# Kernel optimization log

Measured on AMD Instinct MI355X. Metric: run time of the kernel, lower is better.

Reference implementation:

```python
import jax, jax.numpy as jnp
import numpy as np

# dims
B, S, D, H, L = 4, 2048, 512, 8, 4
DH = D // H          # head dim 64
MLP = 2048
VOCAB = 32000
BLK = 128            # block size
NB = S // BLK        # 16 blocks
SINK_ITERS = 8       # sinkhorn normalization iterations
NEG = -1e9


def _sinusoid_pos_emb(max_len, d):
    pos = np.arange(max_len, dtype=np.float32)[:, None]
    div = np.exp(np.arange(0, d, 2, dtype=np.float32) * (-np.log(10000.0) / d))
    pe = np.zeros((max_len, d), np.float32)
    pe[:, 0::2] = np.sin(pos * div)
    pe[:, 1::2] = np.cos(pos * div)
    return pe

_PE = jnp.asarray(_sinusoid_pos_emb(S, D))


def setup_inputs() -> dict:
    key = jax.random.key(0)
    ks = jax.random.split(key, 12)
    g = lambda k, shape, s=0.02: jax.random.normal(k, shape, jnp.float32) * s
    tokens = jax.random.randint(ks[0], (B, S), 0, VOCAB)
    return {
        "tokens": tokens,
        "embed": g(ks[1], (VOCAB, D), 1.0),
        "ln1_s": jnp.ones((L, D)), "ln1_b": jnp.zeros((L, D)),
        "wq": g(ks[2], (L, D, H, DH)),
        "wk": g(ks[3], (L, D, H, DH)),
        "wv": g(ks[4], (L, D, H, DH)),
        "wo": g(ks[5], (L, H, DH, D)),
        "sort_w": g(ks[6], (L, H, DH, NB)),
        "ln2_s": jnp.ones((L, D)), "ln2_b": jnp.zeros((L, D)),
        "w1": g(ks[7], (L, D, MLP)), "b1": jnp.zeros((L, MLP)),
        "w2": g(ks[8], (L, MLP, D)), "b2": jnp.zeros((L, D)),
        "lnf_s": jnp.ones((D,)), "lnf_b": jnp.zeros((D,)),
    }


def _ln(x, s, b):
    m = jnp.mean(x, axis=-1, keepdims=True)
    v = jnp.mean(jnp.square(x - m), axis=-1, keepdims=True)
    return (x - m) * jax.lax.rsqrt(v + 1e-6) * s + b


def _sinkhorn(log_alpha):
    # iterative row/col normalization in log space -> soft permutation
    for _ in range(SINK_ITERS):
        log_alpha = log_alpha - jax.nn.logsumexp(log_alpha, axis=-1, keepdims=True)
        log_alpha = log_alpha - jax.nn.logsumexp(log_alpha, axis=-2, keepdims=True)
    return jnp.exp(log_alpha)


def _forward(tokens, embed, ln1_s, ln1_b, wq, wk, wv, wo, sort_w,
             ln2_s, ln2_b, w1, b1, w2, b2, lnf_s, lnf_b):
    pad = (tokens > 0)                       # [B,S] key padding mask
    mb = pad.reshape(B, NB, BLK).astype(jnp.float32)  # block mask
    x = embed[tokens] + _PE[None, :S]        # [B,S,D]
    scale = 1.0 / jnp.sqrt(jnp.float32(DH))
    for l in range(L):
        h = _ln(x, ln1_s[l], ln1_b[l])
        q = jnp.einsum('bsd,dhf->bshf', h, wq[l]) * scale
        k = jnp.einsum('bsd,dhf->bshf', h, wk[l])
        v = jnp.einsum('bsd,dhf->bshf', h, wv[l])
        qb = q.reshape(B, NB, BLK, H, DH)
        kb = k.reshape(B, NB, BLK, H, DH)
        vb = v.reshape(B, NB, BLK, H, DH)
        # sort net: block summary of keys -> block-to-block logits per head
        ksum = kb.sum(axis=2)                               # [B,NB,H,DH]
        logits = jnp.einsum('bnhd,hdm->bhnm', ksum, sort_w[l])
        perm = _sinkhorn(logits)                            # [B,H,NB,NB]
        sk = jnp.einsum('bhnm,bmchd->bnchd', perm, kb)      # sorted key blocks
        sv = jnp.einsum('bhnm,bmchd->bnchd', perm, vb)
        kcat = jnp.concatenate([kb, sk], axis=2)            # [B,NB,2BLK,H,DH]
        vcat = jnp.concatenate([vb, sv], axis=2)
        scores = jnp.einsum('bnqhd,bnkhd->bhnqk', qb, kcat)  # [B,H,NB,BLK,2BLK]
        # padding bias: local part from block mask, sorted part via permuted mask
        local = jnp.broadcast_to(mb[:, None, :, None, :], (B, H, NB, 1, BLK))
        smask = (jnp.einsum('bhnm,bmc->bhnc', jax.lax.stop_gradient(perm), mb) > 0.5)
        smask = smask[:, :, :, None, :].astype(jnp.float32)
        full_mask = jnp.concatenate([local, jnp.broadcast_to(smask, (B, H, NB, 1, BLK))], axis=-1)
        scores = scores + jnp.where(full_mask > 0.5, 0.0, NEG)
        attn = jax.nn.softmax(scores, axis=-1)
        o = jnp.einsum('bhnqk,bnkhd->bnqhd', attn, vcat).reshape(B, S, H, DH)
        x = x + jnp.einsum('bshd,hdD->bsD', o, wo[l])
        y = _ln(x, ln2_s[l], ln2_b[l])
        y = jax.nn.gelu(jnp.einsum('bsd,df->bsf', y, w1[l]) + b1[l])
        x = x + jnp.einsum('bsf,fd->bsd', y, w2[l]) + b2[l]
    return _ln(x, lnf_s, lnf_b)


def reference(tokens, embed, ln1_s, ln1_b, wq, wk, wv, wo, sort_w,
              ln2_s, ln2_b, w1, b1, w2, b2, lnf_s, lnf_b):
    return _forward(tokens, embed, ln1_s, ln1_b, wq, wk, wv, wo, sort_w,
                    ln2_s, ln2_b, w1, b1, w2, b2, lnf_s, lnf_b)
```

## Files before the change

### kernel.cpp

```cpp
#include <hip/hip_runtime.h>
#include <math.h>

#define B_ 4
#define S_ 2048
#define D_ 512
#define H_ 8
#define L_ 4
#define DH_ 64
#define MLP_ 2048
#define BLK_ 128
#define NB_ 16
#define NEGINF -1e9f
#define NXE ((size_t)B_ * S_ * D_)

typedef unsigned short u16;
typedef __attribute__((ext_vector_type(8))) short short8;
typedef __attribute__((ext_vector_type(4))) short short4v;
typedef __attribute__((ext_vector_type(4))) float f32x4;

__device__ __forceinline__ float bf2f(u16 s) {
  return __uint_as_float(((unsigned)s) << 16);
}
__device__ __forceinline__ u16 f2bf(float f) {
  unsigned u = __float_as_uint(f);
  unsigned r = (u + 0x7FFFu + ((u >> 16) & 1u)) >> 16;
  return (u16)r;
}

__device__ __forceinline__ void gll16(const void* g, void* l) {
  __builtin_amdgcn_global_load_lds(
      (const __attribute__((address_space(1))) unsigned int*)g,
      (__attribute__((address_space(3))) unsigned int*)l, 16, 0, 0);
}

__global__ __launch_bounds__(128) void k_embed(const int* __restrict__ tokens,
                                               const float* __restrict__ embed,
                                               float* __restrict__ x) {
  int s = blockIdx.x;
  int tid = threadIdx.x;
  const float c = -logf(10000.0f) / (float)D_;
  int d = tid * 4;
  float pe[4];
#pragma unroll
  for (int j = 0; j < 4; ++j) {
    int dd = d + j;
    int i2 = dd >> 1;
    float freq = __expf(c * (float)(2 * i2));
    float ang = (float)s * freq;
    pe[j] = (dd & 1) ? cosf(ang) : sinf(ang);
  }
#pragma unroll
  for (int b = 0; b < B_; ++b) {
    int tok = tokens[b * S_ + s];
    float4 e = *(const float4*)(embed + (size_t)tok * D_ + d);
    *(float4*)(x + (size_t)(b * S_ + s) * D_ + d) =
        make_float4(e.x + pe[0], e.y + pe[1], e.z + pe[2], e.w + pe[3]);
  }
}

template <typename OT>
__global__ __launch_bounds__(256) void k_ln(const float* __restrict__ x,
                                            const float* __restrict__ sc,
                                            const float* __restrict__ bi,
                                            OT* __restrict__ out, int rows) {
  int row = blockIdx.x * 4 + (threadIdx.x >> 6);
  int lane = threadIdx.x & 63;
  if (row >= rows) return;
  const float* xr = x + (size_t)row * D_;
  float v[8];
  float4 a = *(const float4*)(xr + lane * 8);
  float4 b = *(const float4*)(xr + lane * 8 + 4);
  v[0]=a.x; v[1]=a.y; v[2]=a.z; v[3]=a.w; v[4]=b.x; v[5]=b.y; v[6]=b.z; v[7]=b.w;
  float sum = 0.f;
#pragma unroll
  for (int j = 0; j < 8; ++j) sum += v[j];
#pragma unroll
  for (int off = 32; off; off >>= 1) sum += __shfl_xor(sum, off);
  float mean = sum * (1.0f / D_);
  float var = 0.f;
#pragma unroll
  for (int j = 0; j < 8; ++j) { float d = v[j] - mean; var += d * d; }
#pragma unroll
  for (int off = 32; off; off >>= 1) var += __shfl_xor(var, off);
  float rstd = rsqrtf(var * (1.0f / D_) + 1e-6f);
  float o[8];
#pragma unroll
  for (int j = 0; j < 8; ++j) {
    int d = lane * 8 + j;
    o[j] = (v[j] - mean) * rstd * sc[d] + bi[d];
  }
  if constexpr (sizeof(OT) == 4) {
    float* op = (float*)out + (size_t)row * D_ + lane * 8;
    *(float4*)op = make_float4(o[0], o[1], o[2], o[3]);
    *(float4*)(op + 4) = make_float4(o[4], o[5], o[6], o[7]);
  } else {
    u16* op = (u16*)out + (size_t)row * D_ + lane * 8;
    short8 o8;
#pragma unroll
    for (int j = 0; j < 8; ++j) o8[j] = (short)f2bf(o[j]);
    *(short8*)op = o8;
  }
}

__global__ __launch_bounds__(256) void k_transp(const float* __restrict__ W,
                                                u16* __restrict__ WT, int K, int N,
                                                size_t wStrideZ, size_t tStrideZ) {
  __shared__ float t[32][33];
  const float* Wl = W + (size_t)blockIdx.z * wStrideZ;
  u16* WTl = WT + (size_t)blockIdx.z * tStrideZ;
  int k0 = blockIdx.x * 32, n0 = blockIdx.y * 32;
  int x = threadIdx.x & 31, y = threadIdx.x >> 5;
#pragma unroll
  for (int yy = y; yy < 32; yy += 8)
    t[yy][x] = Wl[(size_t)(k0 + yy) * N + n0 + x];
  __syncthreads();
#pragma unroll
  for (int yy = y; yy < 32; yy += 8)
    WTl[(size_t)(n0 + yy) * K + k0 + x] = f2bf(t[x][yy]);
}

__device__ __forceinline__ float gelu_f(float x) {
  float y = 0.7978845608028654f * (x + 0.044715f * x * x * x);
  float e = __expf(2.0f * y);
  return x - x / (e + 1.0f);
}

enum { EPI_STORE = 0, EPI_ADD = 1, EPI_GELU = 2, EPI_ADDBIAS = 3, EPI_QKV = 4 };

template <int EPI>
__device__ __forceinline__ void epilogue_elem(u16* Cb, float* Cf, float bv,
                                              int row, int col, int N, float alpha,
                                              float v) {
  if (EPI == EPI_STORE) {
    Cb[(size_t)row * N + col] = f2bf(v * alpha);
  } else if (EPI == EPI_QKV) {
    u16* dst = Cb + (size_t)(col >> 9) * NXE;
    float al = (col < 512) ? alpha : 1.0f;
    dst[(size_t)row * D_ + (col & 511)] = f2bf(v * al);
  } else if (EPI == EPI_GELU) {
    Cb[(size_t)row * N + col] = f2bf(gelu_f(v + bv));
  } else if (EPI == EPI_ADD) {
    Cf[(size_t)row * N + col] += v;
  } else {
    Cf[(size_t)row * N + col] += v + bv;
  }
}

template <int EPI>
__global__ __launch_bounds__(256) void k_mm(const u16* __restrict__ A,
                                            const u16* __restrict__ BT,
                                            const float* __restrict__ bias,
                                            u16* __restrict__ Cb,
                                            float* __restrict__ Cf,
                                            int M, int N, int K, float alpha) {
  __shared__ u16 Al[2][128 * 32];
  __shared__ u16 Bl[2][128 * 32];
  int tid = threadIdx.x;
  int lane = tid & 63;
  int wave = tid >> 6;
  int nwg = gridDim.x * gridDim.y;
  int bid = blockIdx.y * gridDim.x + blockIdx.x;
  int cpx = nwg >> 3;
  int swz = (bid & 7) * cpx + (bid >> 3);
  int bx = swz % gridDim.x, by = swz / gridDim.x;
  int m0 = by * 128, n0 = bx * 128;
  int wm = (wave >> 1) * 64, wn = (wave & 1) * 64;
  int l15 = lane & 15, l4 = lane >> 4;

  int schunk = (tid & 3) ^ ((tid >> 3) & 3);
  const u16* Ag0 = A + (size_t)(m0 + (tid >> 2)) * K + schunk * 8;
  const u16* Ag1 = Ag0 + (size_t)64 * K;
  const u16* Bg0 = BT + (size_t)(n0 + (tid >> 2)) * K + schunk * 8;
  const u16* Bg1 = Bg0 + (size_t)64 * K;

  auto stage = [&](int buf, int kt) {
    int k0 = kt * 32;
    char* AlB = (char*)(&Al[buf][0]) + wave * 1024;
    char* BlB = (char*)(&Bl[buf][0]) + wave * 1024;
    gll16(Ag0 + k0, AlB);
    gll16(Ag1 + k0, AlB + 4096);
    gll16(Bg0 + k0, BlB);
    gll16(Bg1 + k0, BlB + 4096);
  };

  f32x4 zero = {0.f, 0.f, 0.f, 0.f};
  f32x4 acc[4][4];
#pragma unroll
  for (int i = 0; i < 4; ++i)
#pragma unroll
    for (int j = 0; j < 4; ++j) acc[i][j] = zero;

  int NK = K >> 5;
  stage(0, 0);
  asm volatile("s_waitcnt vmcnt(0)" ::: "memory");
  __syncthreads();

  int rchunk = (l4 ^ ((l15 >> 1) & 3)) * 8;

  for (int t = 0; t < NK; ++t) {
    if (t + 1 < NK) stage((t + 1) & 1, t + 1);
    const u16* Ab = &Al[t & 1][0];
    const u16* Bb = &Bl[t & 1][0];
    short8 af[4], bf4[4];
#pragma unroll
    for (int i = 0; i < 4; ++i)
      af[i] = *(const short8*)(Ab + (wm + i * 16 + l15) * 32 + rchunk);
#pragma unroll
    for (int j = 0; j < 4; ++j)
      bf4[j] = *(const short8*)(Bb + (wn + j * 16 + l15) * 32 + rchunk);
#pragma unroll
    for (int i = 0; i < 4; ++i)
#pragma unroll
      for (int j = 0; j < 4; ++j)
        acc[i][j] = __builtin_amdgcn_mfma_f32_16x16x32_bf16(af[i], bf4[j], acc[i][j], 0, 0, 0);
    asm volatile("s_waitcnt vmcnt(0)" ::: "memory");
    __syncthreads();
  }

#pragma unroll
  for (int i = 0; i < 4; ++i)
#pragma unroll
    for (int j = 0; j < 4; ++j) {
      int col = n0 + wn + j * 16 + l15;
      float bv = (EPI == EPI_GELU || EPI == EPI_ADDBIAS) ? bias[col] : 0.f;
#pragma unroll
      for (int r = 0; r < 4; ++r) {
        int row = m0 + wm + i * 16 + l4 * 4 + r;
        epilogue_elem<EPI>(Cb, Cf, bv, row, col, N, alpha, acc[i][j][r]);
      }
    }
}

template <int EPI>
__global__ __launch_bounds__(256) void k_mm64(const u16* __restrict__ A,
                                              const u16* __restrict__ BT,
                                              const float* __restrict__ bias,
                                              u16* __restrict__ Cb,
                                              float* __restrict__ Cf,
                                              int M, int N, int K, float alpha) {
  __shared__ u16 Al[2][64 * 64];
  __shared__ u16 Bl[2][64 * 64];
  int tid = threadIdx.x;
  int lane = tid & 63;
  int wave = tid >> 6;
  int nwg = gridDim.x * gridDim.y;
  int bid = blockIdx.y * gridDim.x + blockIdx.x;
  int cpx = nwg >> 3;
  int swz = (bid & 7) * cpx + (bid >> 3);
  int bx = swz % gridDim.x, by = swz / gridDim.x;
  int m0 = by * 64, n0 = bx * 64;
  int wm = (wave >> 1) * 32, wn = (wave & 1) * 32;
  int l15 = lane & 15, l4 = lane >> 4;

  int row0 = tid >> 3;
  int lchunk = (tid & 7) ^ (row0 & 7);
  const u16* Ag0 = A + (size_t)(m0 + row0) * K + lchunk * 8;
  const u16* Ag1 = Ag0 + (size_t)32 * K;
  const u16* Bg0 = BT + (size_t)(n0 + row0) * K + lchunk * 8;
  const u16* Bg1 = Bg0 + (size_t)32 * K;

  auto stage = [&](int buf, int kt) {
    int k0 = kt * 64;
    char* AlB = (char*)(&Al[buf][0]) + (wave * 64) * 16;
    char* BlB = (char*)(&Bl[buf][0]) + (wave * 64) * 16;
    gll16(Ag0 + k0, AlB);
    gll16(Ag1 + k0, AlB + 256 * 16);
    gll16(Bg0 + k0, BlB);
    gll16(Bg1 + k0, BlB + 256 * 16);
  };

  f32x4 zero = {0.f, 0.f, 0.f, 0.f};
  f32x4 acc[2][2];
#pragma unroll
  for (int i = 0; i < 2; ++i)
#pragma unroll
    for (int j = 0; j < 2; ++j) acc[i][j] = zero;

  int NK = K >> 6;
  stage(0, 0);
  asm volatile("s_waitcnt vmcnt(0)" ::: "memory");
  __syncthreads();

  for (int t = 0; t < NK; ++t) {
    if (t + 1 < NK) stage((t + 1) & 1, t + 1);
    const u16* Ab = &Al[t & 1][0];
    const u16* Bb = &Bl[t & 1][0];
    short8 af[2][2], bf4[2][2];
#pragma unroll
    for (int i = 0; i < 2; ++i) {
      int ar = wm + i * 16 + l15;
#pragma unroll
      for (int ks = 0; ks < 2; ++ks)
        af[i][ks] = *(const short8*)(Ab + ar * 64 + (((ks * 4 + l4) ^ (ar & 7))) * 8);
    }
#pragma unroll
    for (int j = 0; j < 2; ++j) {
      int br = wn + j * 16 + l15;
#pragma unroll
      for (int ks = 0; ks < 2; ++ks)
        bf4[j][ks] = *(const short8*)(Bb + br * 64 + (((ks * 4 + l4) ^ (br & 7))) * 8);
    }
#pragma unroll
    for (int ks = 0; ks < 2; ++ks)
#pragma unroll
      for (int i = 0; i < 2; ++i)
#pragma unroll
        for (int j = 0; j < 2; ++j)
          acc[i][j] = __builtin_amdgcn_mfma_f32_16x16x32_bf16(af[i][ks], bf4[j][ks], acc[i][j], 0, 0, 0);
    asm volatile("s_waitcnt vmcnt(0)" ::: "memory");
    __syncthreads();
  }

#pragma unroll
  for (int i = 0; i < 2; ++i)
#pragma unroll
    for (int j = 0; j < 2; ++j) {
      int col = n0 + wn + j * 16 + l15;
      float bv = (EPI == EPI_GELU || EPI == EPI_ADDBIAS) ? bias[col] : 0.f;
#pragma unroll
      for (int r = 0; r < 4; ++r) {
        int row = m0 + wm + i * 16 + l4 * 4 + r;
        epilogue_elem<EPI>(Cb, Cf, bv, row, col, N, alpha, acc[i][j][r]);
      }
    }
}

__global__ __launch_bounds__(256) void k_sort(const u16* __restrict__ K,
                                              const float* __restrict__ sortw_l,
                                              const int* __restrict__ tokens,
                                              float* __restrict__ PM,
                                              float* __restrict__ SM) {
  int bh = blockIdx.x;
  int h = bh & (H_ - 1), b = bh >> 3;
  int tid = threadIdx.x;
  __shared__ float ks[NB_][DH_];
  __shared__ float mbm[NB_][BLK_];
  __shared__ float buf[256];
  __shared__ float red[16];

  for (int it = tid; it < S_; it += 256)
    mbm[it >> 7][it & 127] = (tokens[b * S_ + it] > 0) ? 1.f : 0.f;

  if (tid < 128) {
    int n = tid >> 3, ch = (tid & 7) * 8;
    const u16* kp = K + (((size_t)(b * S_ + n * BLK_) * H_) + h) * DH_ + ch;
    float s[8] = {};
    for (int c = 0; c < BLK_; ++c) {
      short8 v = *(const short8*)(kp + (size_t)c * (H_ * DH_));
#pragma unroll
      for (int j = 0; j < 8; ++j) s[j] += bf2f((u16)v[j]);
    }
#pragma unroll
    for (int j = 0; j < 8; ++j) ks[n][ch + j] = s[j];
  }
  __syncthreads();

  int n = tid >> 4, m = tid & 15;
  const float* wp = sortw_l + (size_t)h * DH_ * NB_;
  float la = 0.f;
#pragma unroll
  for (int d = 0; d < DH_; ++d) la += ks[n][d] * wp[d * NB_ + m];

  for (int it = 0; it < 8; ++it) {
    buf[tid] = la;
    __syncthreads();
    if (m == 0) {
      float mx = buf[n * 16];
      for (int t = 1; t < 16; ++t) mx = fmaxf(mx, buf[n * 16 + t]);
      float s = 0.f;
      for (int t = 0; t < 16; ++t) s += __expf(buf[n * 16 + t] - mx);
      red[n] = mx + __logf(s);
    }
    __syncthreads();
    la -= red[n];
    buf[tid] = la;
    __syncthreads();
    if (tid < 16) {
      float mx = buf[tid];
      for (int t = 1; t < 16; ++t) mx = fmaxf(mx, buf[t * 16 + tid]);
      float s = 0.f;
      for (int t = 0; t < 16; ++t) s += __expf(buf[t * 16 + tid] - mx);
      red[tid] = mx + __logf(s);
    }
    __syncthreads();
    la -= red[m];
    __syncthreads();
  }
  float pm = __expf(la);
  PM[(size_t)bh * 256 + tid] = pm;
  buf[tid] = pm;
  __syncthreads();

  for (int it = tid; it < NB_ * BLK_; it += 256) {
    int nn = it >> 7, c = it & 127;
    float s = 0.f;
#pragma unroll
    for (int mm = 0; mm < NB_; ++mm) s += buf[nn * 16 + mm] * mbm[mm][c];
    SM[(size_t)bh * (NB_ * BLK_) + it] = s;
  }
}

__global__ __launch_bounds__(256) void k_sortblocks(
    const float* __restrict__ perm, const u16* __restrict__ K,
    const u16* __restrict__ V,
    u16* __restrict__ SK, u16* __restrict__ SV) {
  int n = blockIdx.x, h = blockIdx.y, b = blockIdx.z;
  int tid = threadIdx.x;
  __shared__ float pr[NB_];
  if (tid < NB_) pr[tid] = perm[(((size_t)(b * H_ + h) * NB_) + n) * NB_ + tid];
  __syncthreads();
  for (int it = tid; it < 1024; it += 256) {
    int c = it >> 3;
    int f8 = (it & 7) * 8;
    float ak[8] = {}, av[8] = {};
#pragma unroll
    for (int m = 0; m < NB_; ++m) {
      float p = pr[m];
      size_t off = (((size_t)(b * S_ + m * BLK_ + c) * H_) + h) * DH_ + f8;
      short8 kv = *(const short8*)(K + off);
      short8 vv = *(const short8*)(V + off);
#pragma unroll
      for (int j = 0; j < 8; ++j) {
        ak[j] += p * bf2f((u16)kv[j]);
        av[j] += p * bf2f((u16)vv[j]);
      }
    }
    short8 ok, ov;
#pragma unroll
    for (int j = 0; j < 8; ++j) {
      ok[j] = (short)f2bf(ak[j]);
      ov[j] = (short)f2bf(av[j]);
    }
    size_t oo = (((size_t)(b * S_ + n * BLK_ + c) * H_) + h) * DH_ + f8;
    *(short8*)(SK + oo) = ok;
    *(short8*)(SV + oo) = ov;
  }
}

__global__ __launch_bounds__(512) void k_attn(
    const u16* __restrict__ Q, const u16* __restrict__ Kg, const u16* __restrict__ SK,
    const u16* __restrict__ Vg, const u16* __restrict__ SV,
    const int* __restrict__ tokens, const float* __restrict__ smask,
    u16* __restrict__ O) {
  int n = blockIdx.x, h = blockIdx.y, b = blockIdx.z;
  int tid = threadIdx.x;
  int lane = tid & 63;
  int w = tid >> 6;
  int l15 = lane & 15, l4 = lane >> 4;

  __shared__ u16 KV[16384];
  __shared__ u16 Pl[32768];
  __shared__ float sbias[256];

  short8 vreg[4];
  int vrow;
  {
    vrow = tid & 255;
    int rl = vrow & 127;
    const u16* vsrc = (vrow < BLK_) ? Vg : SV;
    const u16* vbase = vsrc + (((size_t)(b * S_ + n * BLK_ + rl) * H_) + h) * DH_;
    int fh = (tid >> 8) * 8;
#pragma unroll
    for (int s = 0; s < 4; ++s)
      vreg[s] = *(const short8*)(vbase + s * 16 + fh);
  }

#pragma unroll
  for (int s = 0; s < 4; ++s) {
    int c = s * 512 + tid;
    int r = c >> 3;
    int fs = (c & 7) ^ (r & 7);
    const u16* ksrc = (r < BLK_) ? Kg : SK;
    gll16(ksrc + (((size_t)(b * S_ + n * BLK_ + (r & 127)) * H_) + h) * DH_ + fs * 8,
          (char*)KV + (s * 512 + w * 64) * 16);
  }

  short8 qf0, qf1;
  {
    const u16* qp = Q + (((size_t)(b * S_ + n * BLK_ + w * 16 + l15) * H_) + h) * DH_ + l4 * 8;
    qf0 = *(const short8*)(qp);
    qf1 = *(const short8*)(qp + 32);
  }

  if (tid < 256) {
    float mval = (tid < BLK_)
        ? ((tokens[b * S_ + n * BLK_ + tid] > 0) ? 1.f : 0.f)
        : smask[(((size_t)(b * H_ + h) * NB_) + n) * BLK_ + (tid - BLK_)];
    sbias[tid] = (mval > 0.5f) ? 0.f : NEGINF;
  }
  __syncthreads();

  f32x4 zero = {0.f, 0.f, 0.f, 0.f};
  f32x4 st[16];
#pragma unroll
  for (int m = 0; m < 16; ++m) st[m] = zero;
#pragma unroll
  for (int m = 0; m < 16; ++m) {
    int arow = m * 16 + l15;
    const u16* kb = KV + arow * 64;
    int sw = arow & 7;
    short8 a0 = *(const short8*)(kb + ((l4 ^ sw) * 8));
    short8 a1 = *(const short8*)(kb + (((4 + l4) ^ sw) * 8));
    st[m] = __builtin_amdgcn_mfma_f32_16x16x32_bf16(a0, qf0, st[m], 0, 0, 0);
    st[m] = __builtin_amdgcn_mfma_f32_16x16x32_bf16(a1, qf1, st[m], 0, 0, 0);
  }

  float mx = -3.0e38f;
#pragma unroll
  for (int m = 0; m < 16; ++m)
#pragma unroll
    for (int r = 0; r < 4; ++r) {
      st[m][r] += sbias[m * 16 + l4 * 4 + r];
      mx = fmaxf(mx, st[m][r]);
    }
  mx = fmaxf(mx, __shfl_xor(mx, 16));
  mx = fmaxf(mx, __shfl_xor(mx, 32));
  float sum = 0.f;
#pragma unroll
  for (int m = 0; m < 16; ++m)
#pragma unroll
    for (int r = 0; r < 4; ++r) {
      float e = __expf(st[m][r] - mx);
      st[m][r] = e;
      sum += e;
    }
  sum += __shfl_xor(sum, 16);
  sum += __shfl_xor(sum, 32);
  float inv = 1.0f / sum;

  int q = w * 16 + l15;
  int qx = q & 31;
#pragma unroll
  for (int m = 0; m < 16; ++m) {
    short4v p4;
#pragma unroll
    for (int r = 0; r < 4; ++r) p4[r] = (short)f2bf(st[m][r] * inv);
    int slot = (m * 4 + l4) ^ qx;
    *(short4v*)(Pl + q * 256 + slot * 4) = p4;
  }
  __syncthreads();

  {
    int fh = (tid >> 8) * 8;
#pragma unroll
    for (int s = 0; s < 4; ++s) {
#pragma unroll
      for (int j = 0; j < 8; ++j) {
        int d = s * 16 + fh + j;
        KV[d * 256 + (((vrow >> 3) ^ (d & 7)) * 8) + (vrow & 7)] = (u16)vreg[s][j];
      }
    }
  }
  __syncthreads();

  f32x4 oacc[4];
#pragma unroll
  for (int nf = 0; nf < 4; ++nf) oacc[nf] = zero;
#pragma unroll
  for (int kk = 0; kk < 8; ++kk) {
    int s0 = (kk * 8 + l4 * 2) ^ qx;
    int s1 = (kk * 8 + l4 * 2 + 1) ^ qx;
    short4v a0 = *(const short4v*)(Pl + q * 256 + s0 * 4);
    short4v a1 = *(const short4v*)(Pl + q * 256 + s1 * 4);
    short8 af;
#pragma unroll
    for (int j = 0; j < 4; ++j) { af[j] = a0[j]; af[4 + j] = a1[j]; }
#pragma unroll
    for (int nf = 0; nf < 4; ++nf) {
      int d = nf * 16 + l15;
      short8 bf = *(const short8*)(KV + d * 256 + (((kk * 4 + l4) ^ (d & 7)) * 8));
      oacc[nf] = __builtin_amdgcn_mfma_f32_16x16x32_bf16(af, bf, oacc[nf], 0, 0, 0);
    }
  }

  u16* ob = O + (((size_t)(b * S_ + n * BLK_) * H_) + h) * DH_;
#pragma unroll
  for (int nf = 0; nf < 4; ++nf) {
    int d = nf * 16 + l15;
#pragma unroll
    for (int r = 0; r < 4; ++r) {
      int qq = w * 16 + l4 * 4 + r;
      ob[(size_t)qq * (H_ * DH_) + d] = f2bf(oacc[nf][r]);
    }
  }
}

extern "C" void kernel_launch(void* const* d_in, const int* in_sizes, int n_in,
                              void* d_out, int out_size, void* d_ws, size_t ws_size,
                              hipStream_t stream) {
  const int* tokens = (const int*)d_in[0];
  const float* embed = (const float*)d_in[1];
  const float* ln1_s = (const float*)d_in[2];
  const float* ln1_b = (const float*)d_in[3];
  const float* wq = (const float*)d_in[4];
  const float* wk = (const float*)d_in[5];
  const float* wv = (const float*)d_in[6];
  const float* wo = (const float*)d_in[7];
  const float* sortw = (const float*)d_in[8];
  const float* ln2_s = (const float*)d_in[9];
  const float* ln2_b = (const float*)d_in[10];
  const float* w1 = (const float*)d_in[11];
  const float* b1 = (const float*)d_in[12];
  const float* w2 = (const float*)d_in[13];
  const float* b2 = (const float*)d_in[14];
  const float* lnf_s = (const float*)d_in[15];
  const float* lnf_b = (const float*)d_in[16];
  float* out = (float*)d_out;

  const size_t NX = NXE;
  float* ws = (float*)d_ws;
  float* X = ws;
  float* ATT = ws + NX;
  u16* HID = (u16*)ATT;
  u16* Hbf = (u16*)(ws + 5 * NX);
  u16* Qb = Hbf + NX;
  u16* Kb = Qb + NX;
  u16* Vb = Kb + NX;
  u16* SKb = Vb + NX;
  u16* SVb = SKb + NX;
  u16* Ob = Hbf;
  float* PM = (float*)(SVb + NX);
  float* SM = PM + (size_t)B_ * H_ * NB_ * NB_;
  u16* WT = (u16*)(SM + (size_t)B_ * H_ * NB_ * BLK_);
  u16* wqkvT = WT;
  u16* woT = wqkvT + (size_t)L_ * 3 * D_ * D_;
  u16* w1T = woT + (size_t)L_ * D_ * D_;
  u16* w2T = w1T + (size_t)L_ * D_ * MLP_;

  const int rows = B_ * S_;
  const float scale = 0.125f;
  const size_t qkvStride = (size_t)3 * D_ * D_;

  k_transp<<<dim3(16, 16, L_), 256, 0, stream>>>(wq, wqkvT, D_, D_, (size_t)D_ * D_, qkvStride);
  k_transp<<<dim3(16, 16, L_), 256, 0, stream>>>(wk, wqkvT + (size_t)512 * 512, D_, D_, (size_t)D_ * D_, qkvStride);
  k_transp<<<dim3(16, 16, L_), 256, 0, stream>>>(wv, wqkvT + (size_t)1024 * 512, D_, D_, (size_t)D_ * D_, qkvStride);
  k_transp<<<dim3(16, 16, L_), 256, 0, stream>>>(wo, woT, D_, D_, (size_t)D_ * D_, (size_t)D_ * D_);
  k_transp<<<dim3(16, 64, L_), 256, 0, stream>>>(w1, w1T, D_, MLP_, (size_t)D_ * MLP_, (size_t)MLP_ * D_);
  k_transp<<<dim3(64, 16, L_), 256, 0, stream>>>(w2, w2T, MLP_, D_, (size_t)MLP_ * D_, (size_t)D_ * MLP_);

  k_embed<<<S_, 128, 0, stream>>>(tokens, embed, X);

  for (int l = 0; l < L_; ++l) {
    k_ln<u16><<<rows / 4, 256, 0, stream>>>(X, ln1_s + l * D_, ln1_b + l * D_, Hbf, rows);
    dim3 gqkv(1536 / 64, rows / 64);
    k_mm64<EPI_QKV><<<gqkv, 256, 0, stream>>>(Hbf, wqkvT + (size_t)l * qkvStride, nullptr, Qb, nullptr, rows, 1536, D_, scale);
    k_sort<<<B_ * H_, 256, 0, stream>>>(Kb, sortw + (size_t)l * H_ * DH_ * NB_, tokens, PM, SM);
    dim3 gatt(NB_, H_, B_);
    k_sortblocks<<<gatt, 256, 0, stream>>>(PM, Kb, Vb, SKb, SVb);
    k_attn<<<gatt, 512, 0, stream>>>(Qb, Kb, SKb, Vb, SVb, tokens, SM, Ob);
    dim3 go(D_ / 64, rows / 64);
    k_mm64<EPI_ADD><<<go, 256, 0, stream>>>(Ob, woT + (size_t)l * D_ * D_, nullptr, nullptr, X, rows, D_, D_, 1.0f);
    k_ln<u16><<<rows / 4, 256, 0, stream>>>(X, ln2_s + l * D_, ln2_b + l * D_, Hbf, rows);
    dim3 g2(MLP_ / 128, rows / 128);
    k_mm<EPI_GELU><<<g2, 256, 0, stream>>>(Hbf, w1T + (size_t)l * D_ * MLP_, b1 + (size_t)l * MLP_, HID, nullptr, rows, MLP_, D_, 1.0f);
    dim3 g3(D_ / 64, rows / 64);
    k_mm64<EPI_ADDBIAS><<<g3, 256, 0, stream>>>(HID, w2T + (size_t)l * MLP_ * D_, b2 + (size_t)l * D_, nullptr, X, rows, D_, MLP_, 1.0f);
  }
  k_ln<float><<<rows / 4, 256, 0, stream>>>(X, lnf_s, lnf_b, out, rows);
}
```

Measured before the change: 767.8 us.

## Fuse block-sort mixing into attention kernel and use 64-tile GEMM for MLP up-projection

The separate sort-blocks kernel, which wrote permuted K/V to global buffers, is removed. The attention kernel now computes the soft-permuted K and V blocks itself from the permutation matrix and stages them straight into shared memory, which saves a launch and a global write and read of two activation-sized buffers. The MLP first GEMM also switches from the 128x128 tile kernel to the 64x64 tile kernel. The trade-off is that each attention workgroup now does the 16-block weighted sum inline, which adds latency per block, and the smaller tiles give less data reuse on the large GEMM.

```diff
diff --git a/kernel.cpp b/kernel.cpp
--- a/kernel.cpp
+++ b/kernel.cpp
@@ -144,91 +144,6 @@
   } else {
     Cf[(size_t)row * N + col] += v + bv;
   }
-}
-
-template <int EPI>
-__global__ __launch_bounds__(256) void k_mm(const u16* __restrict__ A,
-                                            const u16* __restrict__ BT,
-                                            const float* __restrict__ bias,
-                                            u16* __restrict__ Cb,
-                                            float* __restrict__ Cf,
-                                            int M, int N, int K, float alpha) {
-  __shared__ u16 Al[2][128 * 32];
-  __shared__ u16 Bl[2][128 * 32];
-  int tid = threadIdx.x;
-  int lane = tid & 63;
-  int wave = tid >> 6;
-  int nwg = gridDim.x * gridDim.y;
-  int bid = blockIdx.y * gridDim.x + blockIdx.x;
-  int cpx = nwg >> 3;
-  int swz = (bid & 7) * cpx + (bid >> 3);
-  int bx = swz % gridDim.x, by = swz / gridDim.x;
-  int m0 = by * 128, n0 = bx * 128;
-  int wm = (wave >> 1) * 64, wn = (wave & 1) * 64;
-  int l15 = lane & 15, l4 = lane >> 4;
-
-  int schunk = (tid & 3) ^ ((tid >> 3) & 3);
-  const u16* Ag0 = A + (size_t)(m0 + (tid >> 2)) * K + schunk * 8;
-  const u16* Ag1 = Ag0 + (size_t)64 * K;
-  const u16* Bg0 = BT + (size_t)(n0 + (tid >> 2)) * K + schunk * 8;
-  const u16* Bg1 = Bg0 + (size_t)64 * K;
-
-  auto stage = [&](int buf, int kt) {
-    int k0 = kt * 32;
-    char* AlB = (char*)(&Al[buf][0]) + wave * 1024;
-    char* BlB = (char*)(&Bl[buf][0]) + wave * 1024;
-    gll16(Ag0 + k0, AlB);
-    gll16(Ag1 + k0, AlB + 4096);
-    gll16(Bg0 + k0, BlB);
-    gll16(Bg1 + k0, BlB + 4096);
-  };
-
-  f32x4 zero = {0.f, 0.f, 0.f, 0.f};
-  f32x4 acc[4][4];
-#pragma unroll
-  for (int i = 0; i < 4; ++i)
-#pragma unroll
-    for (int j = 0; j < 4; ++j) acc[i][j] = zero;
-
-  int NK = K >> 5;
-  stage(0, 0);
-  asm volatile("s_waitcnt vmcnt(0)" ::: "memory");
-  __syncthreads();
-
-  int rchunk = (l4 ^ ((l15 >> 1) & 3)) * 8;
-
-  for (int t = 0; t < NK; ++t) {
-    if (t + 1 < NK) stage((t + 1) & 1, t + 1);
-    const u16* Ab = &Al[t & 1][0];
-    const u16* Bb = &Bl[t & 1][0];
-    short8 af[4], bf4[4];
-#pragma unroll
-    for (int i = 0; i < 4; ++i)
-      af[i] = *(const short8*)(Ab + (wm + i * 16 + l15) * 32 + rchunk);
-#pragma unroll
-    for (int j = 0; j < 4; ++j)
-      bf4[j] = *(const short8*)(Bb + (wn + j * 16 + l15) * 32 + rchunk);
-#pragma unroll
-    for (int i = 0; i < 4; ++i)
-#pragma unroll
-      for (int j = 0; j < 4; ++j)
-        acc[i][j] = __builtin_amdgcn_mfma_f32_16x16x32_bf16(af[i], bf4[j], acc[i][j], 0, 0, 0);
-    asm volatile("s_waitcnt vmcnt(0)" ::: "memory");
-    __syncthreads();
-  }
-
-#pragma unroll
-  for (int i = 0; i < 4; ++i)
-#pragma unroll
-    for (int j = 0; j < 4; ++j) {
-      int col = n0 + wn + j * 16 + l15;
-      float bv = (EPI == EPI_GELU || EPI == EPI_ADDBIAS) ? bias[col] : 0.f;
-#pragma unroll
-      for (int r = 0; r < 4; ++r) {
-        int row = m0 + wm + i * 16 + l4 * 4 + r;
-        epilogue_elem<EPI>(Cb, Cf, bv, row, col, N, alpha, acc[i][j][r]);
-      }
-    }
 }
 
 template <int EPI>
@@ -400,48 +315,10 @@
   }
 }
 
-__global__ __launch_bounds__(256) void k_sortblocks(
-    const float* __restrict__ perm, const u16* __restrict__ K,
-    const u16* __restrict__ V,
-    u16* __restrict__ SK, u16* __restrict__ SV) {
-  int n = blockIdx.x, h = blockIdx.y, b = blockIdx.z;
-  int tid = threadIdx.x;
-  __shared__ float pr[NB_];
-  if (tid < NB_) pr[tid] = perm[(((size_t)(b * H_ + h) * NB_) + n) * NB_ + tid];
-  __syncthreads();
-  for (int it = tid; it < 1024; it += 256) {
-    int c = it >> 3;
-    int f8 = (it & 7) * 8;
-    float ak[8] = {}, av[8] = {};
-#pragma unroll
-    for (int m = 0; m < NB_; ++m) {
-      float p = pr[m];
-      size_t off = (((size_t)(b * S_ + m * BLK_ + c) * H_) + h) * DH_ + f8;
-      short8 kv = *(const short8*)(K + off);
-      short8 vv = *(const short8*)(V + off);
-#pragma unroll
-      for (int j = 0; j < 8; ++j) {
-        ak[j] += p * bf2f((u16)kv[j]);
-        av[j] += p * bf2f((u16)vv[j]);
-      }
-    }
-    short8 ok, ov;
-#pragma unroll
-    for (int j = 0; j < 8; ++j) {
-      ok[j] = (short)f2bf(ak[j]);
-      ov[j] = (short)f2bf(av[j]);
-    }
-    size_t oo = (((size_t)(b * S_ + n * BLK_ + c) * H_) + h) * DH_ + f8;
-    *(short8*)(SK + oo) = ok;
-    *(short8*)(SV + oo) = ov;
-  }
-}
-
 __global__ __launch_bounds__(512) void k_attn(
-    const u16* __restrict__ Q, const u16* __restrict__ Kg, const u16* __restrict__ SK,
-    const u16* __restrict__ Vg, const u16* __restrict__ SV,
-    const int* __restrict__ tokens, const float* __restrict__ smask,
-    u16* __restrict__ O) {
+    const u16* __restrict__ Q, const u16* __restrict__ Kg, const u16* __restrict__ Vg,
+    const float* __restrict__ PMg, const int* __restrict__ tokens,
+    const float* __restrict__ smask, u16* __restrict__ O) {
   int n = blockIdx.x, h = blockIdx.y, b = blockIdx.z;
   int tid = threadIdx.x;
   int lane = tid & 63;
@@ -451,27 +328,14 @@
   __shared__ u16 KV[16384];
   __shared__ u16 Pl[32768];
   __shared__ float sbias[256];
-
-  short8 vreg[4];
-  int vrow;
-  {
-    vrow = tid & 255;
-    int rl = vrow & 127;
-    const u16* vsrc = (vrow < BLK_) ? Vg : SV;
-    const u16* vbase = vsrc + (((size_t)(b * S_ + n * BLK_ + rl) * H_) + h) * DH_;
-    int fh = (tid >> 8) * 8;
-#pragma unroll
-    for (int s = 0; s < 4; ++s)
-      vreg[s] = *(const short8*)(vbase + s * 16 + fh);
-  }
-
-#pragma unroll
-  for (int s = 0; s < 4; ++s) {
+  __shared__ float prs[NB_];
+
+#pragma unroll
+  for (int s = 0; s < 2; ++s) {
     int c = s * 512 + tid;
     int r = c >> 3;
     int fs = (c & 7) ^ (r & 7);
-    const u16* ksrc = (r < BLK_) ? Kg : SK;
-    gll16(ksrc + (((size_t)(b * S_ + n * BLK_ + (r & 127)) * H_) + h) * DH_ + fs * 8,
+    gll16(Kg + (((size_t)(b * S_ + n * BLK_ + r) * H_) + h) * DH_ + fs * 8,
           (char*)KV + (s * 512 + w * 64) * 16);
   }
 
@@ -482,11 +346,66 @@
     qf1 = *(const short8*)(qp + 32);
   }
 
+  int vr = tid >> 2, vq = (tid & 3) * 16;
+  short8 vloc[2];
+  {
+    const u16* vbase = Vg + (((size_t)(b * S_ + n * BLK_ + vr) * H_) + h) * DH_ + vq;
+    vloc[0] = *(const short8*)(vbase);
+    vloc[1] = *(const short8*)(vbase + 8);
+  }
+
+  if (tid < NB_) prs[tid] = PMg[(((size_t)(b * H_ + h) * NB_) + n) * NB_ + tid];
   if (tid < 256) {
     float mval = (tid < BLK_)
         ? ((tokens[b * S_ + n * BLK_ + tid] > 0) ? 1.f : 0.f)
         : smask[(((size_t)(b * H_ + h) * NB_) + n) * BLK_ + (tid - BLK_)];
     sbias[tid] = (mval > 0.5f) ? 0.f : NEGINF;
+  }
+  __syncthreads();
+
+#pragma unroll
+  for (int s = 0; s < 2; ++s) {
+    int c = 1024 + s * 512 + tid;
+    int r = c >> 3;
+    int rs = r & 127;
+    int p = c & 7;
+    int ls = p ^ (r & 7);
+    const u16* kp = Kg + (((size_t)(b * S_ + rs) * H_) + h) * DH_ + ls * 8;
+    float ak[8] = {};
+#pragma unroll
+    for (int m = 0; m < NB_; ++m) {
+      float pr = prs[m];
+      short8 kv = *(const short8*)(kp + (size_t)m * (BLK_ * H_ * DH_));
+#pragma unroll
+      for (int j = 0; j < 8; ++j) ak[j] += pr * bf2f((u16)kv[j]);
+    }
+    short8 ok;
+#pragma unroll
+    for (int j = 0; j < 8; ++j) ok[j] = (short)f2bf(ak[j]);
+    *(short8*)(KV + r * 64 + p * 8) = ok;
+  }
+
+  short8 vsrt[2];
+  {
+    const u16* vp = Vg + (((size_t)(b * S_ + vr) * H_) + h) * DH_ + vq;
+    float av[16] = {};
+#pragma unroll
+    for (int m = 0; m < NB_; ++m) {
+      float pr = prs[m];
+      const u16* vm = vp + (size_t)m * (BLK_ * H_ * DH_);
+      short8 v0 = *(const short8*)(vm);
+      short8 v1 = *(const short8*)(vm + 8);
+#pragma unroll
+      for (int j = 0; j < 8; ++j) {
+        av[j] += pr * bf2f((u16)v0[j]);
+        av[8 + j] += pr * bf2f((u16)v1[j]);
+      }
+    }
+#pragma unroll
+    for (int j = 0; j < 8; ++j) {
+      vsrt[0][j] = (short)f2bf(av[j]);
+      vsrt[1][j] = (short)f2bf(av[8 + j]);
+    }
   }
   __syncthreads();
 
@@ -540,16 +459,22 @@
   }
   __syncthreads();
 
+#pragma unroll
+  for (int half = 0; half < 2; ++half)
+#pragma unroll
+    for (int j = 0; j < 8; ++j) {
+      int d = vq + half * 8 + j;
+      KV[d * 256 + (((vr >> 3) ^ (d & 7)) * 8) + (vr & 7)] = (u16)vloc[half][j];
+    }
   {
-    int fh = (tid >> 8) * 8;
-#pragma unroll
-    for (int s = 0; s < 4; ++s) {
+    int r2 = vr + 128;
+#pragma unroll
+    for (int half = 0; half < 2; ++half)
 #pragma unroll
       for (int j = 0; j < 8; ++j) {
-        int d = s * 16 + fh + j;
-        KV[d * 256 + (((vrow >> 3) ^ (d & 7)) * 8) + (vrow & 7)] = (u16)vreg[s][j];
+        int d = vq + half * 8 + j;
+        KV[d * 256 + (((r2 >> 3) ^ (d & 7)) * 8) + (r2 & 7)] = (u16)vsrt[half][j];
       }
-    }
   }
   __syncthreads();
 
@@ -616,10 +541,8 @@
   u16* Qb = Hbf + NX;
   u16* Kb = Qb + NX;
   u16* Vb = Kb + NX;
-  u16* SKb = Vb + NX;
-  u16* SVb = SKb + NX;
   u16* Ob = Hbf;
-  float* PM = (float*)(SVb + NX);
+  float* PM = (float*)(Vb + NX);
   float* SM = PM + (size_t)B_ * H_ * NB_ * NB_;
   u16* WT = (u16*)(SM + (size_t)B_ * H_ * NB_ * BLK_);
   u16* wqkvT = WT;
@@ -646,13 +569,12 @@
     k_mm64<EPI_QKV><<<gqkv, 256, 0, stream>>>(Hbf, wqkvT + (size_t)l * qkvStride, nullptr, Qb, nullptr, rows, 1536, D_, scale);
     k_sort<<<B_ * H_, 256, 0, stream>>>(Kb, sortw + (size_t)l * H_ * DH_ * NB_, tokens, PM, SM);
     dim3 gatt(NB_, H_, B_);
-    k_sortblocks<<<gatt, 256, 0, stream>>>(PM, Kb, Vb, SKb, SVb);
-    k_attn<<<gatt, 512, 0, stream>>>(Qb, Kb, SKb, Vb, SVb, tokens, SM, Ob);
+    k_attn<<<gatt, 512, 0, stream>>>(Qb, Kb, Vb, PM, tokens, SM, Ob);
     dim3 go(D_ / 64, rows / 64);
     k_mm64<EPI_ADD><<<go, 256, 0, stream>>>(Ob, woT + (size_t)l * D_ * D_, nullptr, nullptr, X, rows, D_, D_, 1.0f);
     k_ln<u16><<<rows / 4, 256, 0, stream>>>(X, ln2_s + l * D_, ln2_b + l * D_, Hbf, rows);
-    dim3 g2(MLP_ / 128, rows / 128);
-    k_mm<EPI_GELU><<<g2, 256, 0, stream>>>(Hbf, w1T + (size_t)l * D_ * MLP_, b1 + (size_t)l * MLP_, HID, nullptr, rows, MLP_, D_, 1.0f);
+    dim3 g2(MLP_ / 64, rows / 64);
+    k_mm64<EPI_GELU><<<g2, 256, 0, stream>>>(Hbf, w1T + (size_t)l * D_ * MLP_, b1 + (size_t)l * MLP_, HID, nullptr, rows, MLP_, D_, 1.0f);
     dim3 g3(D_ / 64, rows / 64);
     k_mm64<EPI_ADDBIAS><<<g3, 256, 0, stream>>>(HID, w2T + (size_t)l * MLP_ * D_, b2 + (size_t)l * D_, nullptr, X, rows, D_, MLP_, 1.0f);
   }
```

Measured after the change: 737.9 us. 3.9% less time.
